# Performance work log

Measured on AMD Instinct MI355X. Metric: run time of the kernel, lower is better.

The kernel has to match this reference:

```python
import jax, jax.numpy as jnp
import numpy as np

K, PAD, STRIDE, TREE_DEPTH = 3, 1, 1, 3


def _unfold(x, k, pad, stride):
    # torch.nn.Unfold, channel-major feature ordering: feat = c*k*k + (ki*k+kj)
    B, C, H, W = x.shape
    Ho = (H + 2 * pad - k) // stride + 1
    Wo = (W + 2 * pad - k) // stride + 1
    xp = jnp.pad(x, ((0, 0), (0, 0), (pad, pad), (pad, pad)))
    cols = [xp[:, :, ki:ki + stride * Ho:stride, kj:kj + stride * Wo:stride]
            for ki in range(k) for kj in range(k)]
    p = jnp.stack(cols, axis=2)               # [B, C, k*k, Ho, Wo]
    p = p.reshape(B, C * k * k, Ho * Wo)      # [B, C*k*k, L]
    return p.transpose(0, 2, 1), Ho, Wo       # [B, L, C*k*k]


def _bin_ops(a, b):
    # the 16 soft binary logic gates, stacked on a trailing axis
    ab = a * b
    s = a + b
    zero = jnp.zeros_like(a)
    one = jnp.ones_like(a)
    return jnp.stack([zero, ab, a - ab, a, b - ab, b,
                      s - 2 * ab, s - ab, 1 - (s - ab), 1 - (s - 2 * ab),
                      1 - b, 1 - b + ab, 1 - a, 1 - a + ab, 1 - ab, one], axis=-1)


def setup_inputs() -> dict:
    key = jax.random.key(0)
    k1, k2 = jax.random.split(key)
    B, C_in, H, W = 16, 64, 32, 32
    C_out = 128
    x = jax.random.uniform(k1, (B, C_in, H, W), dtype=jnp.float32)
    weights = jax.random.normal(k2, (C_out, 2 ** TREE_DEPTH - 1, 16), dtype=jnp.float32)
    # replicate the module's leaf-index construction: 2 random channels,
    # 4 random spatial taps each, flattened as c*patch_size + spatial
    rng = np.random.default_rng(0)
    idx = []
    for _ in range(C_out):
        chans = rng.permutation(C_in)[:2]
        parts = [c * (K * K) + rng.permutation(K * K)[:2 ** TREE_DEPTH // 2] for c in chans]
        idx.append(np.concatenate(parts))
    leaf_indices = jnp.asarray(np.stack(idx), dtype=jnp.int32)  # [C_out, 8]
    return {"x": x, "weights": weights, "leaf_indices": leaf_indices}


def reference(x, weights, leaf_indices):
    patches, Ho, Wo = _unfold(x, K, PAD, STRIDE)          # [B, L, C*9]
    # gather the 8 leaf inputs for every output channel at once
    leaves = jnp.take(patches, leaf_indices, axis=2)      # [B, L, O, 8]
    cur = leaves
    for level in range(TREE_DEPTH):
        npairs = cur.shape[-1] // 2
        # faithful to source: gate_idx = 2**level - 1 + pair (indices overlap across levels)
        gate_ids = 2 ** level - 1 + jnp.arange(npairs)
        w = jax.nn.softmax(weights[:, gate_ids], axis=-1)  # [O, npairs, 16]
        a = cur[..., 0::2]
        b = cur[..., 1::2]
        ops = _bin_ops(a, b)                               # [B, L, O, npairs, 16]
        cur = jnp.einsum('blopg,opg->blop', ops, w)        # [B, L, O, npairs]
    out = cur[..., 0]                                      # [B, L, O]
    B = x.shape[0]
    return out.transpose(0, 2, 1).reshape(B, weights.shape[0], Ho, Wo)
```

## Files before the change

kernel.cpp:

```cpp
#include <hip/hip_runtime.h>


#define C_OUT 128
#define C_IN  64
#define HW    32
#define NGATE 4

__device__ __forceinline__ float gate_eval(float4 c, float a, float b) {
    return fmaf(a * b, c.w, fmaf(a, c.y, fmaf(b, c.z, c.x)));
}

__global__ void prep_coeffs(const float* __restrict__ w, float* __restrict__ coef) {
    int t = blockIdx.x * blockDim.x + threadIdx.x;
    if (t >= C_OUT * NGATE) return;
    int o = t >> 2, g = t & 3;
    const float* wp = w + (o * 7 + g) * 16;
    float v[16];
    float m = -1e30f;
    #pragma unroll
    for (int i = 0; i < 16; ++i) { v[i] = wp[i]; m = fmaxf(m, v[i]); }
    float s = 0.f;
    #pragma unroll
    for (int i = 0; i < 16; ++i) { v[i] = expf(v[i] - m); s += v[i]; }
    float inv = 1.f / s;
    #pragma unroll
    for (int i = 0; i < 16; ++i) v[i] *= inv;
    float c0  = v[8] + v[9] + v[10] + v[11] + v[12] + v[13] + v[14] + v[15];
    float ca  = v[2] + v[3] + v[6] + v[7] - v[8] - v[9] - v[12] - v[13];
    float cb  = v[4] + v[5] + v[6] + v[7] - v[8] - v[9] - v[10] - v[11];
    float cab = v[1] - v[2] - v[4] - 2.f * v[6] - v[7] + v[8] + 2.f * v[9]
              + v[11] + v[13] - v[14];
    ((float4*)coef)[t] = make_float4(c0, ca, cb, cab);
}

__global__ __launch_bounds__(1024) void logic_tree(
    const float* __restrict__ x, const int* __restrict__ leaf_idx,
    const float* __restrict__ coef, float* __restrict__ out)
{
    int blk = blockIdx.x;
    int b = blk >> 7;
    int o = blk & (C_OUT - 1);
    int pix = threadIdx.x;
    int h = pix >> 5, w = pix & (HW - 1);

    int cch[8], dy[8], dx[8];
    #pragma unroll
    for (int j = 0; j < 8; ++j) {
        int li = leaf_idx[o * 8 + j];
        int c = li / 9;
        int kk = li - c * 9;
        int ky = kk / 3;
        cch[j] = c;
        dy[j] = ky - 1;
        dx[j] = (kk - ky * 3) - 1;
    }
    float4 cf0 = ((const float4*)coef)[o * 4 + 0];
    float4 cf1 = ((const float4*)coef)[o * 4 + 1];
    float4 cf2 = ((const float4*)coef)[o * 4 + 2];
    float4 cf3 = ((const float4*)coef)[o * 4 + 3];

    const float* xb = x + (size_t)b * C_IN * HW * HW;
    float v[8];
    #pragma unroll
    for (int j = 0; j < 8; ++j) {
        int hh = h + dy[j], ww = w + dx[j];
        bool ok = ((unsigned)hh < HW) & ((unsigned)ww < HW);
        v[j] = ok ? xb[(cch[j] * HW + hh) * HW + ww] : 0.f;
    }

    float p0 = gate_eval(cf0, v[0], v[1]);
    float p1 = gate_eval(cf1, v[2], v[3]);
    float p2 = gate_eval(cf2, v[4], v[5]);
    float p3 = gate_eval(cf3, v[6], v[7]);
    float q0 = gate_eval(cf1, p0, p1);
    float q1 = gate_eval(cf2, p2, p3);
    float r = gate_eval(cf3, q0, q1);

    out[((size_t)b * C_OUT + o) * (HW * HW) + pix] = r;
}

extern "C" void kernel_launch(void* const* d_in, const int* in_sizes, int n_in,
                              void* d_out, int out_size, void* d_ws, size_t ws_size,
                              hipStream_t stream) {
    const float* x       = (const float*)d_in[0];
    const float* weights = (const float*)d_in[1];
    const int*   leaves  = (const int*)d_in[2];
    float* out  = (float*)d_out;
    float* coef = (float*)d_ws;

    prep_coeffs<<<2, 256, 0, stream>>>(weights, coef);
    logic_tree<<<16 * C_OUT, 1024, 0, stream>>>(x, leaves, coef, out);
}
```

Measured before the change: 70.75 us.

## Fuse softmax coefficient prep into tree kernel and process four pixels per thread

Removes the separate coefficient-prep launch: each block now computes its own four softmax-reduced gate coefficients into shared memory, with one barrier before use. Each thread now handles four consecutive pixels using unaligned float4 row loads with edge shifting and zero fill, and writes a float4 result, so blocks shrink from 1024 to 256 threads. This trades a kernel launch and scalar memory traffic for redundant per-block softmax work (2048 blocks each recomputing) and more register pressure and shuffling per thread.

```diff
diff --git a/kernel.cpp b/kernel.cpp
--- a/kernel.cpp
+++ b/kernel.cpp
@@ -4,79 +4,98 @@
 #define C_OUT 128
 #define C_IN  64
 #define HW    32
-#define NGATE 4
 
-__device__ __forceinline__ float gate_eval(float4 c, float a, float b) {
-    return fmaf(a * b, c.w, fmaf(a, c.y, fmaf(b, c.z, c.x)));
+__device__ __forceinline__ float4 ld4u(const float* p) {
+    float4 v;
+    __builtin_memcpy(&v, p, sizeof(float4));
+    return v;
 }
 
-__global__ void prep_coeffs(const float* __restrict__ w, float* __restrict__ coef) {
-    int t = blockIdx.x * blockDim.x + threadIdx.x;
-    if (t >= C_OUT * NGATE) return;
-    int o = t >> 2, g = t & 3;
-    const float* wp = w + (o * 7 + g) * 16;
-    float v[16];
-    float m = -1e30f;
-    #pragma unroll
-    for (int i = 0; i < 16; ++i) { v[i] = wp[i]; m = fmaxf(m, v[i]); }
-    float s = 0.f;
-    #pragma unroll
-    for (int i = 0; i < 16; ++i) { v[i] = expf(v[i] - m); s += v[i]; }
-    float inv = 1.f / s;
-    #pragma unroll
-    for (int i = 0; i < 16; ++i) v[i] *= inv;
-    float c0  = v[8] + v[9] + v[10] + v[11] + v[12] + v[13] + v[14] + v[15];
-    float ca  = v[2] + v[3] + v[6] + v[7] - v[8] - v[9] - v[12] - v[13];
-    float cb  = v[4] + v[5] + v[6] + v[7] - v[8] - v[9] - v[10] - v[11];
-    float cab = v[1] - v[2] - v[4] - 2.f * v[6] - v[7] + v[8] + 2.f * v[9]
-              + v[11] + v[13] - v[14];
-    ((float4*)coef)[t] = make_float4(c0, ca, cb, cab);
+__device__ __forceinline__ float4 gate4(const float4 c, const float4 a, const float4 b) {
+    float4 r;
+    r.x = fmaf(a.x * b.x, c.w, fmaf(a.x, c.y, fmaf(b.x, c.z, c.x)));
+    r.y = fmaf(a.y * b.y, c.w, fmaf(a.y, c.y, fmaf(b.y, c.z, c.x)));
+    r.z = fmaf(a.z * b.z, c.w, fmaf(a.z, c.y, fmaf(b.z, c.z, c.x)));
+    r.w = fmaf(a.w * b.w, c.w, fmaf(a.w, c.y, fmaf(b.w, c.z, c.x)));
+    return r;
 }
 
-__global__ __launch_bounds__(1024) void logic_tree(
-    const float* __restrict__ x, const int* __restrict__ leaf_idx,
-    const float* __restrict__ coef, float* __restrict__ out)
+__global__ __launch_bounds__(256) void logic_tree_fused(
+    const float* __restrict__ x, const float* __restrict__ wts,
+    const int* __restrict__ leaf_idx, float* __restrict__ out)
 {
-    int blk = blockIdx.x;
-    int b = blk >> 7;
-    int o = blk & (C_OUT - 1);
-    int pix = threadIdx.x;
-    int h = pix >> 5, w = pix & (HW - 1);
+    const int blk = blockIdx.x;
+    const int b = blk >> 7;
+    const int o = blk & (C_OUT - 1);
 
-    int cch[8], dy[8], dx[8];
+    __shared__ float4 cf_s[4];
+    if (threadIdx.x < 4) {
+        const int g = threadIdx.x;
+        const float* wp = wts + (o * 7 + g) * 16;
+        float v[16];
+        float m = -1e30f;
+        #pragma unroll
+        for (int i = 0; i < 16; ++i) { v[i] = wp[i]; m = fmaxf(m, v[i]); }
+        float s = 0.f;
+        #pragma unroll
+        for (int i = 0; i < 16; ++i) { v[i] = expf(v[i] - m); s += v[i]; }
+        float inv = 1.f / s;
+        #pragma unroll
+        for (int i = 0; i < 16; ++i) v[i] *= inv;
+        float c0  = v[8]+v[9]+v[10]+v[11]+v[12]+v[13]+v[14]+v[15];
+        float ca  = v[2]+v[3]+v[6]+v[7]-v[8]-v[9]-v[12]-v[13];
+        float cb  = v[4]+v[5]+v[6]+v[7]-v[8]-v[9]-v[10]-v[11];
+        float cab = v[1]-v[2]-v[4]-2.f*v[6]-v[7]+v[8]+2.f*v[9]+v[11]+v[13]-v[14];
+        cf_s[g] = make_float4(c0, ca, cb, cab);
+    }
+
+    int cch[8], dy[8], dxx[8];
     #pragma unroll
     for (int j = 0; j < 8; ++j) {
         int li = leaf_idx[o * 8 + j];
         int c = li / 9;
         int kk = li - c * 9;
         int ky = kk / 3;
-        cch[j] = c;
-        dy[j] = ky - 1;
-        dx[j] = (kk - ky * 3) - 1;
+        cch[j] = c; dy[j] = ky - 1; dxx[j] = (kk - ky * 3) - 1;
     }
-    float4 cf0 = ((const float4*)coef)[o * 4 + 0];
-    float4 cf1 = ((const float4*)coef)[o * 4 + 1];
-    float4 cf2 = ((const float4*)coef)[o * 4 + 2];
-    float4 cf3 = ((const float4*)coef)[o * 4 + 3];
+    __syncthreads();
 
+    const int q = threadIdx.x & 7;
+    const int h = threadIdx.x >> 3;
     const float* xb = x + (size_t)b * C_IN * HW * HW;
-    float v[8];
+
+    float4 v[8];
     #pragma unroll
     for (int j = 0; j < 8; ++j) {
-        int hh = h + dy[j], ww = w + dx[j];
-        bool ok = ((unsigned)hh < HW) & ((unsigned)ww < HW);
-        v[j] = ok ? xb[(cch[j] * HW + hh) * HW + ww] : 0.f;
+        int hh = h + dy[j];
+        bool hok = ((unsigned)hh < HW);
+        const float* rp = xb + (cch[j] * HW + (hok ? hh : 0)) * HW;
+        float4 t;
+        if (dxx[j] == 0) {
+            t = ld4u(rp + 4 * q);
+        } else {
+            int base = 4 * q + dxx[j];
+            int cb = min(max(base, 0), HW - 4);
+            float4 u = ld4u(rp + cb);
+            if (base < 0)            t = make_float4(0.f, u.x, u.y, u.z);
+            else if (base > HW - 4)  t = make_float4(u.y, u.z, u.w, 0.f);
+            else                     t = u;
+        }
+        if (!hok) t = make_float4(0.f, 0.f, 0.f, 0.f);
+        v[j] = t;
     }
 
-    float p0 = gate_eval(cf0, v[0], v[1]);
-    float p1 = gate_eval(cf1, v[2], v[3]);
-    float p2 = gate_eval(cf2, v[4], v[5]);
-    float p3 = gate_eval(cf3, v[6], v[7]);
-    float q0 = gate_eval(cf1, p0, p1);
-    float q1 = gate_eval(cf2, p2, p3);
-    float r = gate_eval(cf3, q0, q1);
+    const float4 cf0 = cf_s[0], cf1 = cf_s[1], cf2 = cf_s[2], cf3 = cf_s[3];
+    float4 p0 = gate4(cf0, v[0], v[1]);
+    float4 p1 = gate4(cf1, v[2], v[3]);
+    float4 p2 = gate4(cf2, v[4], v[5]);
+    float4 p3 = gate4(cf3, v[6], v[7]);
+    float4 q0 = gate4(cf1, p0, p1);
+    float4 q1 = gate4(cf2, p2, p3);
+    float4 r  = gate4(cf3, q0, q1);
 
-    out[((size_t)b * C_OUT + o) * (HW * HW) + pix] = r;
+    float4* op = (float4*)(out + (size_t)(b * C_OUT + o) * (HW * HW));
+    op[threadIdx.x] = r;
 }
 
 extern "C" void kernel_launch(void* const* d_in, const int* in_sizes, int n_in,
@@ -85,9 +104,6 @@
     const float* x       = (const float*)d_in[0];
     const float* weights = (const float*)d_in[1];
     const int*   leaves  = (const int*)d_in[2];
-    float* out  = (float*)d_out;
-    float* coef = (float*)d_ws;
-
-    prep_coeffs<<<2, 256, 0, stream>>>(weights, coef);
-    logic_tree<<<16 * C_OUT, 1024, 0, stream>>>(x, leaves, coef, out);
+    float* out = (float*)d_out;
+    logic_tree_fused<<<16 * C_OUT, 256, 0, stream>>>(x, weights, leaves, out);
 }
```

New measurement: 68.71 us. -2.9%, faster.
